# Optimization experiments

Hardware: AMD Instinct MI355X
Metric: run time of the kernel (lower is better)

Reference implementation:

```python
import jax, jax.numpy as jnp
import numpy as np

DIM = 256; K = 3; PAD = 1; DIL = 1; B = 16; H = 56; W = 56
SP = 8           # share_planes
RADIX = 2
ATTN = max(DIM * RADIX // 4, 32)   # 128
EMB = K * K * DIM // SP            # 288

def conv(x, w, pad=0, dil=1, groups=1):
    return jax.lax.conv_general_dilated(
        x, w, (1, 1), [(pad, pad), (pad, pad)], rhs_dilation=(dil, dil),
        feature_group_count=groups, dimension_numbers=('NCHW', 'OIHW', 'NCHW'))

def bn(x, g, b, m, v, eps=1e-5):
    # eval-mode BatchNorm2d
    s = g * jax.lax.rsqrt(v + eps)
    return x * s[None, :, None, None] + (b - m * s)[None, :, None, None]

def gn(x, g, b, groups, eps=1e-5):
    Bb, C, Hh, Ww = x.shape
    xg = x.reshape(Bb, groups, C // groups, Hh, Ww)
    mu = xg.mean((2, 3, 4), keepdims=True)
    var = xg.var((2, 3, 4), keepdims=True)
    xg = (xg - mu) * jax.lax.rsqrt(var + eps)
    return xg.reshape(Bb, C, Hh, Ww) * g[None, :, None, None] + b[None, :, None, None]

def unfold3(x):
    # im2col for 3x3, stride 1, pad 1 -> (B, C, K*K, H, W)
    Bb, C, Hh, Ww = x.shape
    p = (K - 1) // 2
    xp = jnp.pad(x, ((0, 0), (0, 0), (p, p), (p, p)))
    return jnp.stack([xp[:, :, i:i + Hh, j:j + Ww] for i in range(K) for j in range(K)], axis=2)

def reference(x, ke_w, ke_g, ke_b, ke_m, ke_v, e1_w, e1_g, e1_b, e1_m, e1_v,
              e2_w, e2_b, gng, gnb, c1_w, c1_g, c1_b, c1_m, c1_v,
              b2_g, b2_b, b2_m, b2_v, s1_w, s1_b, s1_g, s1_bb, s1_m, s1_v,
              s2_w, s2_b):
    Bb = x.shape[0]
    # key embed: grouped kxk conv + BN + ReLU
    k = jax.nn.relu(bn(conv(x, ke_w, pad=PAD, dil=DIL, groups=4), ke_g, ke_b, ke_m, ke_v))
    qk = jnp.concatenate([x, k], axis=1)                     # (B, 2*DIM, H, W)
    # dynamic kernel branch
    wemb = jax.nn.relu(bn(conv(qk, e1_w), e1_g, e1_b, e1_m, e1_v))
    wemb = conv(wemb, e2_w) + e2_b[None, :, None, None]
    wemb = gn(wemb, gng, gnb, DIM // SP)                     # GroupNorm(dim//8 groups)
    wemb = wemb.reshape(Bb, DIM // SP, K * K, H, W)
    # value branch
    xq = bn(conv(x, c1_w), c1_g, c1_b, c1_m, c1_v)
    # local dynamic convolution: per-pixel kernel shared across SP channels
    patches = unfold3(xq).reshape(Bb, DIM // SP, SP, K * K, H, W)
    y = (patches * wemb[:, :, None]).sum(3).reshape(Bb, DIM, H, W)
    y = bn(y, b2_g, b2_b, b2_m, b2_v)
    y = y * jax.nn.sigmoid(y)                                # swish
    # split attention over radix=2 branches (y, k)
    xs = jnp.stack([y, k], axis=2)                           # (B, C, 2, H, W)
    gap = xs.sum(2).mean((2, 3), keepdims=True)              # (B, C, 1, 1)
    a = jax.nn.relu(bn(conv(gap, s1_w) + s1_b[None, :, None, None], s1_g, s1_bb, s1_m, s1_v))
    a = conv(a, s2_w) + s2_b[None, :, None, None]            # (B, 2*C, 1, 1)
    a = jax.nn.softmax(a.reshape(Bb, DIM, RADIX), axis=2)
    out = (xs * a[:, :, :, None, None]).sum(2)
    return out

def setup_inputs():
    key = jax.random.key(0)
    ks = iter(jax.random.split(key, 40))
    def n(shape, s=1.0):
        return jax.random.normal(next(ks), shape, jnp.float32) * s
    def u(shape):
        return jax.random.uniform(next(ks), shape, jnp.float32, minval=0.5, maxval=1.5)
    d = {}
    d['x'] = n((B, DIM, H, W))
    d['ke_w'] = n((DIM, DIM // 4, K, K), 0.05)
    d['ke_g'] = u((DIM,)); d['ke_b'] = n((DIM,), 0.1); d['ke_m'] = n((DIM,), 0.1); d['ke_v'] = u((DIM,))
    d['e1_w'] = n((DIM // 2, 2 * DIM, 1, 1), 0.05)
    d['e1_g'] = u((DIM // 2,)); d['e1_b'] = n((DIM // 2,), 0.1); d['e1_m'] = n((DIM // 2,), 0.1); d['e1_v'] = u((DIM // 2,))
    d['e2_w'] = n((EMB, DIM // 2, 1, 1), 0.05); d['e2_b'] = n((EMB,), 0.1)
    d['gng'] = u((EMB,)); d['gnb'] = n((EMB,), 0.1)
    d['c1_w'] = n((DIM, DIM, 1, 1), 0.05)
    d['c1_g'] = u((DIM,)); d['c1_b'] = n((DIM,), 0.1); d['c1_m'] = n((DIM,), 0.1); d['c1_v'] = u((DIM,))
    d['b2_g'] = u((DIM,)); d['b2_b'] = n((DIM,), 0.1); d['b2_m'] = n((DIM,), 0.1); d['b2_v'] = u((DIM,))
    d['s1_w'] = n((ATTN, DIM, 1, 1), 0.05); d['s1_b'] = n((ATTN,), 0.1)
    d['s1_g'] = u((ATTN,)); d['s1_bb'] = n((ATTN,), 0.1); d['s1_m'] = n((ATTN,), 0.1); d['s1_v'] = u((ATTN,))
    d['s2_w'] = n((RADIX * DIM, ATTN, 1, 1), 0.05); d['s2_b'] = n((RADIX * DIM,), 0.1)
    return d
```

## Files before the change

### kernel.cpp

```cpp
#include <hip/hip_runtime.h>
#include <hip/hip_bf16.h>

typedef __hip_bfloat16 bf16;
typedef float f32x4 __attribute__((ext_vector_type(4)));
typedef short s16x8 __attribute__((ext_vector_type(8)));

#define NPIX 3136
#define HDIM 56
#define CDIM 256
#define PPIX 3364

static __device__ __forceinline__ float b2f(bf16 v){ return __bfloat162float(v); }
static __device__ __forceinline__ bf16  f2b(float v){ return __float2bfloat16(v); }

#define O_KE_S 0
#define O_KE_B 256
#define O_E1_S 512
#define O_E1_B 640
#define O_C1_S 768
#define O_C1_B 1024
#define O_B2_S 1280
#define O_B2_B 1536
#define O_S1_S 1792
#define O_S1_B 1920
#define O_E2B  2048
#define O_GNS  2336
#define O_GAP  3360
#define O_ATT  7456

__global__ void prep(
    const float* __restrict__ kew, const float* __restrict__ e1w,
    const float* __restrict__ e2w, const float* __restrict__ c1w,
    const float* keg, const float* keb, const float* kem, const float* kev,
    const float* e1g, const float* e1b, const float* e1m, const float* e1v,
    const float* e2b,
    const float* c1g, const float* c1b, const float* c1m, const float* c1v,
    const float* b2g, const float* b2b, const float* b2m, const float* b2v,
    const float* s1g, const float* s1bb, const float* s1m, const float* s1v,
    bf16* kewT, bf16* e1wb, bf16* e2wb, bf16* c1wb, float* o,
    bf16* xh, bf16* xq)
{
    int bid = blockIdx.x, t = threadIdx.x;
    if (bid < 576) {
        int i = bid * 256 + t;
        int ci = i & 63, co_l = (i >> 6) & 63;
        int gt = i >> 12;
        int tap = gt % 9, g = gt / 9;
        int co = g * 64 + co_l;
        kewT[i] = f2b(kew[(co * 64 + ci) * 9 + tap]);
    } else if (bid < 832) {
        int i = (bid - 576) * 256 + t; e1wb[i] = f2b(e1w[i]);
    } else if (bid < 976) {
        int i = (bid - 832) * 256 + t; e2wb[i] = f2b(e2w[i]);
    } else if (bid < 1232) {
        int i = (bid - 976) * 256 + t; c1wb[i] = f2b(c1w[i]);
    } else if (bid == 1232) {
        const float eps = 1e-5f;
        {
            float s = keg[t] * rsqrtf(kev[t] + eps);
            o[O_KE_S + t] = s; o[O_KE_B + t] = keb[t] - kem[t] * s;
            s = c1g[t] * rsqrtf(c1v[t] + eps);
            o[O_C1_S + t] = s; o[O_C1_B + t] = c1b[t] - c1m[t] * s;
            s = b2g[t] * rsqrtf(b2v[t] + eps);
            o[O_B2_S + t] = s; o[O_B2_B + t] = b2b[t] - b2m[t] * s;
        }
        if (t < 128) {
            float s = e1g[t] * rsqrtf(e1v[t] + eps);
            o[O_E1_S + t] = s; o[O_E1_B + t] = e1b[t] - e1m[t] * s;
            s = s1g[t] * rsqrtf(s1v[t] + eps);
            o[O_S1_S + t] = s; o[O_S1_B + t] = s1bb[t] - s1m[t] * s;
        }
        for (int i = t; i < 288; i += 256) o[O_E2B + i] = e2b[i];
    } else if (bid < 1253) {
        int j = (bid - 1233) * 256 + t;
        if (j < 1024) o[O_GNS + j] = 0.f;
        else if (j < 5120) o[O_GAP + j - 1024] = 0.f;
    } else {
        int j = (bid - 1253) * 256 + t;
        bf16* arr = (j >= 116736) ? xq : xh;
        int r = j % 116736;
        int img = r / 7296;
        int s = r % 7296;
        int pi = s >> 5, cc = s & 31;
        int pos;
        if (pi < 58)       pos = pi;
        else if (pi < 116) pos = 57 * 58 + (pi - 58);
        else if (pi < 172) pos = (pi - 115) * 58;
        else               pos = (pi - 171) * 58 + 57;
        float4 z = {0.f, 0.f, 0.f, 0.f};
        *(float4*)(arr + ((long)img * PPIX + pos) * 256 + cc * 8) = z;
    }
}

__global__ __launch_bounds__(256) void cvt_x(const float* __restrict__ x, bf16* __restrict__ xh)
{
    int b = blockIdx.z;
    int c0 = blockIdx.y * 64;
    int p0 = blockIdx.x * 64;
    __shared__ bf16 T[64][72];
    int t = threadIdx.x;
    #pragma unroll
    for (int it = 0; it < 4; it++) {
        int slot = t + it * 256;
        int cl = slot >> 4, ch4 = slot & 15;
        float4 v = *(const float4*)(x + ((long)b * CDIM + c0 + cl) * NPIX + p0 + ch4 * 4);
        T[ch4 * 4 + 0][cl] = f2b(v.x);
        T[ch4 * 4 + 1][cl] = f2b(v.y);
        T[ch4 * 4 + 2][cl] = f2b(v.z);
        T[ch4 * 4 + 3][cl] = f2b(v.w);
    }
    __syncthreads();
    #pragma unroll
    for (int it = 0; it < 2; it++) {
        int slot = t + it * 256;
        int p = slot >> 3, cc = slot & 7;
        int pl = p0 + p;
        int h = pl / HDIM, w = pl - h * HDIM;
        *(float4*)(xh + ((long)b * PPIX + (h + 1) * 58 + (w + 1)) * 256 + c0 + cc * 8) = *(const float4*)&T[p][cc * 8];
    }
}

__global__ __launch_bounds__(256, 4) void gconv_mfma(
    const bf16* __restrict__ xp, const bf16* __restrict__ wT,
    const float* __restrict__ scale, const float* __restrict__ bias,
    bf16* __restrict__ kh, float* __restrict__ gap)
{
    int b = blockIdx.z, g = blockIdx.y;
    int h0 = blockIdx.x * 2;
    __shared__ bf16 As[232 * 64];
    int t = threadIdx.x;
    int wv = t >> 6, lane = t & 63, q = lane >> 4, ln = lane & 15;

    #pragma unroll
    for (int i = 0; i < 8; i++) {
        int slot = t + i * 256;
        if (slot < 1856) {
            int pos = slot >> 3, chunkL = slot & 7;
            int ri = pos / 58, ci = pos - ri * 58;
            int chunkg = chunkL ^ (pos & 7);
            float4 v = *(const float4*)(xp + (((long)b * PPIX + (h0 + ri) * 58 + ci) * 256 + g * 64 + chunkg * 8));
            *(float4*)&As[pos * 64 + chunkL * 8] = v;
        }
    }

    int posb[7];
    #pragma unroll
    for (int pt = 0; pt < 7; pt++) {
        int p = pt * 16 + ln;
        int prow = (p >= 56) ? 1 : 0;
        int pcol = p - prow * 56;
        posb[pt] = prow * 58 + pcol + 1;
    }
    const bf16* wbase = wT + ((long)(g * 9) * 64 + wv * 16 + ln) * 64;

    __syncthreads();

    f32x4 acc[7] = {};
    #pragma unroll
    for (int tap = 0; tap < 9; tap++) {
        const int dr = tap / 3;
        const int dc = tap % 3 - 1;
        const bf16* wq = wbase + tap * 64 * 64;
        s16x8 B0 = *(const s16x8*)(wq + q * 8);
        s16x8 B1 = *(const s16x8*)(wq + 32 + q * 8);
        #pragma unroll
        for (int pt = 0; pt < 7; pt++) {
            int pos = posb[pt] + dr * 58 + dc;
            int off0 = pos * 64 + ((q ^ (pos & 7)) * 8);
            s16x8 a0 = *(const s16x8*)&As[off0];
            s16x8 a1 = *(const s16x8*)&As[off0 ^ 32];
            acc[pt] = __builtin_amdgcn_mfma_f32_16x16x32_bf16(a0, B0, acc[pt], 0, 0, 0);
            acc[pt] = __builtin_amdgcn_mfma_f32_16x16x32_bf16(a1, B1, acc[pt], 0, 0, 0);
        }
    }

    __syncthreads();
    bf16* T = As;
    int co = g * 64 + wv * 16 + ln;
    float sc = scale[co], bi = bias[co];
    #pragma unroll
    for (int pt = 0; pt < 7; pt++)
        #pragma unroll
        for (int r = 0; r < 4; r++)
            T[(pt * 16 + q * 4 + r) * 72 + wv * 16 + ln] = f2b(fmaxf(acc[pt][r] * sc + bi, 0.f));
    __syncthreads();
    int pimg0 = blockIdx.x * 112;
    #pragma unroll
    for (int i = 0; i < 4; i++) {
        int slot = t + i * 256;
        if (slot < 896) {
            int row = slot >> 3, cc = slot & 7;
            *(float4*)(kh + ((long)b * NPIX + pimg0 + row) * CDIM + g * 64 + cc * 8) = *(const float4*)&T[row * 72 + cc * 8];
        }
    }
    {
        int co_l = t & 63, rb = t >> 6;
        float s = 0.f;
        #pragma unroll
        for (int r = 0; r < 28; r++) s += b2f(T[(rb * 28 + r) * 72 + co_l]);
        atomicAdd(&gap[b * 256 + g * 64 + co_l], s);
    }
}

__global__ __launch_bounds__(256) void gemm_pair(
    const bf16* __restrict__ e1w, const bf16* __restrict__ c1w,
    const bf16* __restrict__ X0, const bf16* __restrict__ X1,
    const float* __restrict__ fold,
    bf16* __restrict__ Ye1, bf16* __restrict__ Yc1)
{
    int b = blockIdx.z;
    int p0 = blockIdx.x * 64;
    int by = blockIdx.y;
    const bf16* Wt; int K, M, m0; const float *scp, *bip; bf16* Y; bool relu;
    if (by == 0) { Wt = e1w; K = 512; M = 128; m0 = 0;
                   scp = fold + O_E1_S; bip = fold + O_E1_B; Y = Ye1; relu = true; }
    else         { Wt = c1w; K = 256; M = 256; m0 = (by - 1) * 128;
                   scp = fold + O_C1_S; bip = fold + O_C1_B; Y = Yc1; relu = false; }
    const int C0 = 256;

    __shared__ bf16 SH[64 * 72 + 128 * 72];
    bf16* As = SH;
    bf16* Bs = SH + 64 * 72;
    int t = threadIdx.x;
    int wv = t >> 6, lane = t & 63, q = lane >> 4, ln = lane & 15;

    f32x4 acc[4][2] = {};
    for (int k0 = 0; k0 < K; k0 += 64) {
        __syncthreads();
        #pragma unroll
        for (int i = 0; i < 2; i++) {
            int slot = t + i * 256;
            int chunk = slot & 7, row = slot >> 3;
            int ch = k0 + chunk * 8;
            const bf16* src;
            if (ch < C0) {
                long pp = p0 + row;
                long pidx = (long)b * PPIX + pp + 2 * (pp / HDIM) + 59;
                src = X0 + pidx * C0 + ch;
            } else {
                src = X1 + ((long)b * NPIX + p0 + row) * 256 + (ch - C0);
            }
            *(float4*)&As[row * 72 + chunk * 8] = *(const float4*)src;
        }
        #pragma unroll
        for (int i = 0; i < 4; i++) {
            int slot = t + i * 256;
            int chunk = slot & 7, row = slot >> 3;
            *(float4*)&Bs[row * 72 + chunk * 8] = *(const float4*)(Wt + (long)(m0 + row) * K + k0 + chunk * 8);
        }
        __syncthreads();
        #pragma unroll
        for (int kk = 0; kk < 2; kk++) {
            s16x8 a[4];
            #pragma unroll
            for (int pt = 0; pt < 4; pt++)
                a[pt] = *(const s16x8*)&As[(pt * 16 + ln) * 72 + kk * 32 + q * 8];
            #pragma unroll
            for (int mi = 0; mi < 2; mi++) {
                s16x8 bb = *(const s16x8*)&Bs[(wv * 32 + mi * 16 + ln) * 72 + kk * 32 + q * 8];
                #pragma unroll
                for (int pt = 0; pt < 4; pt++)
                    acc[pt][mi] = __builtin_amdgcn_mfma_f32_16x16x32_bf16(a[pt], bb, acc[pt][mi], 0, 0, 0);
            }
        }
    }

    __syncthreads();
    bf16* T = SH;
    #pragma unroll
    for (int mi = 0; mi < 2; mi++) {
        int m = m0 + wv * 32 + mi * 16 + ln;
        float sc = scp[m], bi = bip[m];
        #pragma unroll
        for (int pt = 0; pt < 4; pt++) {
            #pragma unroll
            for (int r = 0; r < 4; r++) {
                float v = acc[pt][mi][r] * sc + bi;
                if (relu) v = fmaxf(v, 0.f);
                T[(pt * 16 + q * 4 + r) * 144 + wv * 32 + mi * 16 + ln] = f2b(v);
            }
        }
    }
    __syncthreads();
    #pragma unroll
    for (int i = 0; i < 4; i++) {
        int slot = t + i * 256;
        int row = slot >> 4, chunk = slot & 15;
        long pp = p0 + row;
        long pidx = (by == 0) ? ((long)b * NPIX + pp)
                              : ((long)b * PPIX + pp + 2 * (pp / HDIM) + 59);
        *(float4*)(Y + pidx * M + m0 + chunk * 8) = *(const float4*)&T[row * 144 + chunk * 8];
    }
}

__global__ __launch_bounds__(256) void mfma_gemm_e2(
    const bf16* __restrict__ Wt, const bf16* __restrict__ X0,
    const float* __restrict__ bias,
    bf16* __restrict__ Y, float* __restrict__ gnsum)
{
    const int K = 128, M = 288;
    int b = blockIdx.z;
    int p0 = blockIdx.x * 64;
    int m0 = blockIdx.y * 128;
    __shared__ bf16 SH[64 * 72 + 128 * 72];
    bf16* As = SH;
    bf16* Bs = SH + 64 * 72;
    __shared__ float gs[64];
    int t = threadIdx.x;
    int wv = t >> 6, lane = t & 63, q = lane >> 4, ln = lane & 15;
    if (t < 64) gs[t] = 0.f;

    f32x4 acc[4][2] = {};
    for (int k0 = 0; k0 < K; k0 += 64) {
        __syncthreads();
        #pragma unroll
        for (int i = 0; i < 2; i++) {
            int slot = t + i * 256;
            int chunk = slot & 7, row = slot >> 3;
            int ch = k0 + chunk * 8;
            *(float4*)&As[row * 72 + chunk * 8] = *(const float4*)(X0 + ((long)b * NPIX + p0 + row) * K + ch);
        }
        #pragma unroll
        for (int i = 0; i < 4; i++) {
            int slot = t + i * 256;
            int chunk = slot & 7, row = slot >> 3;
            int m = m0 + row;
            float4 v = {0.f, 0.f, 0.f, 0.f};
            if (m < M) v = *(const float4*)(Wt + (long)m * K + k0 + chunk * 8);
            *(float4*)&Bs[row * 72 + chunk * 8] = v;
        }
        __syncthreads();
        #pragma unroll
        for (int kk = 0; kk < 2; kk++) {
            s16x8 a[4];
            #pragma unroll
            for (int pt = 0; pt < 4; pt++)
                a[pt] = *(const s16x8*)&As[(pt * 16 + ln) * 72 + kk * 32 + q * 8];
            #pragma unroll
            for (int mi = 0; mi < 2; mi++) {
                s16x8 bb = *(const s16x8*)&Bs[(wv * 32 + mi * 16 + ln) * 72 + kk * 32 + q * 8];
                #pragma unroll
                for (int pt = 0; pt < 4; pt++)
                    acc[pt][mi] = __builtin_amdgcn_mfma_f32_16x16x32_bf16(a[pt], bb, acc[pt][mi], 0, 0, 0);
            }
        }
    }

    __syncthreads();
    bf16* T = SH;
    #pragma unroll
    for (int mi = 0; mi < 2; mi++) {
        int m = m0 + wv * 32 + mi * 16 + ln;
        int mc = (m > M - 1) ? (M - 1) : m;
        float bi = bias[mc];
        float ps = 0.f, pq = 0.f;
        #pragma unroll
        for (int pt = 0; pt < 4; pt++) {
            #pragma unroll
            for (int r = 0; r < 4; r++) {
                float v = acc[pt][mi][r] + bi;
                ps += v; pq += v * v;
                T[(pt * 16 + q * 4 + r) * 144 + wv * 32 + mi * 16 + ln] = f2b(v);
            }
        }
        if (m < M) {
            int grp = m / 9;
            atomicAdd(&gs[grp * 2], ps);
            atomicAdd(&gs[grp * 2 + 1], pq);
        }
    }
    __syncthreads();
    #pragma unroll
    for (int i = 0; i < 4; i++) {
        int slot = t + i * 256;
        int chunk = slot & 15, row = slot >> 4;
        int m = m0 + chunk * 8;
        if (m + 8 <= M)
            *(float4*)(Y + ((long)b * NPIX + p0 + row) * M + m) = *(const float4*)&T[row * 144 + chunk * 8];
    }
    if (t < 64) atomicAdd(&gnsum[b * 64 + t], gs[t]);
}

__global__ __launch_bounds__(256) void dynconv(
    const bf16* __restrict__ xq, const bf16* __restrict__ wemb,
    const float* __restrict__ gnsum,
    const float* __restrict__ gng, const float* __restrict__ gnb,
    const float* __restrict__ b2s, const float* __restrict__ b2b,
    bf16* __restrict__ y, float* __restrict__ gap)
{
    int t = threadIdx.x;
    int grp = t & 31, pl = t >> 5;
    int bid = blockIdx.x;
    int b = bid / 392;
    int p0 = (bid - b * 392) * 8;
    int p = p0 + pl;
    int h = p / HDIM, w = p - h * HDIM;

    __shared__ bf16 WE[2304];
    __shared__ float SA[288], SC[288];
    __shared__ float R[8][256];

    {
        const bf16* src = wemb + (long)(b * NPIX + p0) * 288;
        #pragma unroll
        for (int i = 0; i < 2; i++) {
            int s = t + i * 256;
            if (s < 288) *(float4*)&WE[s * 8] = *(const float4*)(src + s * 8);
        }
    }
    for (int s = t; s < 288; s += 256) {
        int g2 = s / 9;
        float S = gnsum[b * 64 + g2 * 2], Q = gnsum[b * 64 + g2 * 2 + 1];
        float mu = S * (1.f / 28224.f);
        float var = Q * (1.f / 28224.f) - mu * mu;
        float rs = rsqrtf(fmaxf(var, 0.f) + 1e-5f);
        float a = rs * gng[s];
        SA[s] = a;
        SC[s] = gnb[s] - mu * a;
    }
    __syncthreads();

    long base = ((long)b * PPIX + (h + 1) * 58 + (w + 1)) * 256 + grp * 8;
    const bf16* rm = xq + base - 58 * 256;
    const bf16* rc = xq + base;
    const bf16* rq = xq + base + 58 * 256;
    s16x8 xv[9];
    xv[0] = *(const s16x8*)(rm - 256); xv[1] = *(const s16x8*)rm; xv[2] = *(const s16x8*)(rm + 256);
    xv[3] = *(const s16x8*)(rc - 256); xv[4] = *(const s16x8*)rc; xv[5] = *(const s16x8*)(rc + 256);
    xv[6] = *(const s16x8*)(rq - 256); xv[7] = *(const s16x8*)rq; xv[8] = *(const s16x8*)(rq + 256);

    float acc[8] = {};
    #pragma unroll
    for (int tp = 0; tp < 9; tp++) {
        int wi = grp * 9 + tp;
        float wt = b2f(WE[pl * 288 + wi]) * SA[wi] + SC[wi];
        const bf16* xb = (const bf16*)&xv[tp];
        #pragma unroll
        for (int i = 0; i < 8; i++) acc[i] += b2f(xb[i]) * wt;
    }

    bf16 outv[8];
    float sv[8];
    #pragma unroll
    for (int i = 0; i < 8; i++) {
        int c = grp * 8 + i;
        float v = acc[i] * b2s[c] + b2b[c];
        float sw = v / (1.f + __expf(-v));
        sv[i] = sw;
        outv[i] = f2b(sw);
    }
    *(float4*)(y + ((long)b * NPIX + p) * CDIM + grp * 8) = *(const float4*)outv;

    #pragma unroll
    for (int i = 0; i < 8; i++) R[pl][grp * 8 + i] = sv[i];
    __syncthreads();
    float s = 0.f;
    #pragma unroll
    for (int j = 0; j < 8; j++) s += R[j][t];
    atomicAdd(&gap[b * 256 + t], s);
}

__global__ void attnk(const float* __restrict__ gap,
                      const float* __restrict__ s1w, const float* __restrict__ s1b,
                      const float* __restrict__ s1s, const float* __restrict__ s1bi,
                      const float* __restrict__ s2w, const float* __restrict__ s2b,
                      float* __restrict__ att)
{
    int b = blockIdx.x, t = threadIdx.x;
    __shared__ float g[256], a1[128];
    for (int i = t; i < 256; i += 128) g[i] = gap[b * 256 + i] * (1.f / NPIX);
    __syncthreads();
    float s = 0.f;
    for (int ci = 0; ci < 256; ci++) s += s1w[t * 256 + ci] * g[ci];
    s += s1b[t];
    s = s * s1s[t] + s1bi[t];
    a1[t] = fmaxf(s, 0.f);
    __syncthreads();
    for (int c = t; c < 256; c += 128) {
        float v0 = s2b[2 * c], v1 = s2b[2 * c + 1];
        for (int ci = 0; ci < 128; ci++) {
            float av = a1[ci];
            v0 += s2w[(2 * c) * 128 + ci] * av;
            v1 += s2w[(2 * c + 1) * 128 + ci] * av;
        }
        float m = fmaxf(v0, v1);
        float e0 = __expf(v0 - m), e1 = __expf(v1 - m);
        float inv = 1.f / (e0 + e1);
        att[(b * 256 + c) * 2 + 0] = e0 * inv;
        att[(b * 256 + c) * 2 + 1] = e1 * inv;
    }
}

__global__ __launch_bounds__(256) void finalk(
    const bf16* __restrict__ y, const bf16* __restrict__ k,
    const float* __restrict__ att, float* __restrict__ out)
{
    int b = blockIdx.z, c0 = blockIdx.y * 64, p0 = blockIdx.x * 64;
    __shared__ bf16 Ys[64][72], Ks[64][72];
    int t = threadIdx.x;
    #pragma unroll
    for (int i = 0; i < 2; i++) {
        int slot = t + i * 256;
        int row = slot >> 3, cc = slot & 7;
        long off = ((long)b * NPIX + p0 + row) * CDIM + c0 + cc * 8;
        *(float4*)&Ys[row][cc * 8] = *(const float4*)(y + off);
        *(float4*)&Ks[row][cc * 8] = *(const float4*)(k + off);
    }
    __syncthreads();
    int c_l = t >> 2, pc = t & 3;
    int c = c0 + c_l;
    float a0 = att[(b * 256 + c) * 2], a1 = att[(b * 256 + c) * 2 + 1];
    float4 o[4];
    float* of = (float*)o;
    #pragma unroll
    for (int j = 0; j < 16; j++) {
        int p = pc * 16 + j;
        of[j] = b2f(Ys[p][c_l]) * a0 + b2f(Ks[p][c_l]) * a1;
    }
    float* dst = out + ((long)b * CDIM + c) * NPIX + p0 + pc * 16;
    #pragma unroll
    for (int j = 0; j < 4; j++) ((float4*)dst)[j] = o[j];
}

extern "C" void kernel_launch(void* const* d_in, const int* in_sizes, int n_in,
                              void* d_out, int out_size, void* d_ws, size_t ws_size,
                              hipStream_t stream)
{
    const float* x    = (const float*)d_in[0];
    const float* ke_w = (const float*)d_in[1];
    const float* ke_g = (const float*)d_in[2];
    const float* ke_b = (const float*)d_in[3];
    const float* ke_m = (const float*)d_in[4];
    const float* ke_v = (const float*)d_in[5];
    const float* e1_w = (const float*)d_in[6];
    const float* e1_g = (const float*)d_in[7];
    const float* e1_b = (const float*)d_in[8];
    const float* e1_m = (const float*)d_in[9];
    const float* e1_v = (const float*)d_in[10];
    const float* e2_w = (const float*)d_in[11];
    const float* e2_b = (const float*)d_in[12];
    const float* gng  = (const float*)d_in[13];
    const float* gnb  = (const float*)d_in[14];
    const float* c1_w = (const float*)d_in[15];
    const float* c1_g = (const float*)d_in[16];
    const float* c1_b = (const float*)d_in[17];
    const float* c1_m = (const float*)d_in[18];
    const float* c1_v = (const float*)d_in[19];
    const float* b2_g = (const float*)d_in[20];
    const float* b2_b = (const float*)d_in[21];
    const float* b2_m = (const float*)d_in[22];
    const float* b2_v = (const float*)d_in[23];
    const float* s1_w = (const float*)d_in[24];
    const float* s1_b = (const float*)d_in[25];
    const float* s1_g = (const float*)d_in[26];
    const float* s1_bb= (const float*)d_in[27];
    const float* s1_m = (const float*)d_in[28];
    const float* s1_v = (const float*)d_in[29];
    const float* s2_w = (const float*)d_in[30];
    const float* s2_b = (const float*)d_in[31];

    float* fold = (float*)d_ws;
    bf16* wsb   = (bf16*)((char*)d_ws + 65536);
    bf16* xh   = wsb;
    bf16* kh   = xh + 13778944L;
    bf16* wemb = kh + 12845056L;
    bf16* w1   = wemb + 14450688L;
    bf16* kewT = w1 + 6422528L;
    bf16* e1wb = kewT + 147456L;
    bf16* e2wb = e1wb + 65536L;
    bf16* c1wb = e2wb + 36864L;
    bf16* xq   = c1wb + 65536L;
    bf16* yb   = xh;

    prep<<<dim3(2165), dim3(256), 0, stream>>>(
        ke_w, e1_w, e2_w, c1_w,
        ke_g, ke_b, ke_m, ke_v, e1_g, e1_b, e1_m, e1_v, e2_b,
        c1_g, c1_b, c1_m, c1_v, b2_g, b2_b, b2_m, b2_v,
        s1_g, s1_bb, s1_m, s1_v,
        kewT, e1wb, e2wb, c1wb, fold, xh, xq);

    cvt_x<<<dim3(49, 4, 16), dim3(256), 0, stream>>>(x, xh);

    gconv_mfma<<<dim3(28, 4, 16), dim3(256), 0, stream>>>(
        xh, kewT, fold + O_KE_S, fold + O_KE_B, kh, fold + O_GAP);

    gemm_pair<<<dim3(49, 3, 16), dim3(256), 0, stream>>>(
        e1wb, c1wb, xh, kh, fold, w1, xq);

    mfma_gemm_e2<<<dim3(49, 3, 16), dim3(256), 0, stream>>>(
        e2wb, w1, fold + O_E2B, wemb, fold + O_GNS);

    dynconv<<<dim3(6272), dim3(256), 0, stream>>>(
        xq, wemb, fold + O_GNS, gng, gnb,
        fold + O_B2_S, fold + O_B2_B, yb, fold + O_GAP);

    attnk<<<dim3(16), dim3(128), 0, stream>>>(
        fold + O_GAP, s1_w, s1_b, fold + O_S1_S, fold + O_S1_B, s2_w, s2_b, fold + O_ATT);

    finalk<<<dim3(49, 4, 16), dim3(256), 0, stream>>>(yb, kh, fold + O_ATT, (float*)d_out);
}
```

Baseline: 352.5 us.

## Co-schedule grouped conv with c1 GEMM and precompute GroupNorm fold

Merges the grouped 3x3 key conv and the independent c1 1x1 GEMM into one launch, with block-index ranges selecting which role each block plays, so the two run concurrently and fill the GPU better. The e1 GEMM becomes its own specialised kernel. GroupNorm scale/shift is now computed once per batch in a small gnfold kernel rather than recomputed by each of the 6272 dynconv blocks. This adds one extra launch and moves the workspace offset to make room for the folded values. The heterogeneous blocks may also unbalance the schedule.

New measurement: 333.0 us. -5.5%, faster.

```diff
diff --git a/kernel.cpp b/kernel.cpp
--- a/kernel.cpp
+++ b/kernel.cpp
@@ -27,6 +27,7 @@
 #define O_GNS  2336
 #define O_GAP  3360
 #define O_ATT  7456
+#define O_SA   15872
 
 __global__ void prep(
     const float* __restrict__ kew, const float* __restrict__ e1w,
@@ -120,104 +121,164 @@
     }
 }
 
-__global__ __launch_bounds__(256, 4) void gconv_mfma(
+__global__ __launch_bounds__(256) void gconv_c1(
     const bf16* __restrict__ xp, const bf16* __restrict__ wT,
-    const float* __restrict__ scale, const float* __restrict__ bias,
-    bf16* __restrict__ kh, float* __restrict__ gap)
-{
-    int b = blockIdx.z, g = blockIdx.y;
-    int h0 = blockIdx.x * 2;
-    __shared__ bf16 As[232 * 64];
+    const float* __restrict__ kes, const float* __restrict__ keb,
+    const bf16* __restrict__ c1w,
+    const float* __restrict__ c1s, const float* __restrict__ c1b,
+    bf16* __restrict__ kh, bf16* __restrict__ xq, float* __restrict__ gap)
+{
+    __shared__ bf16 SH[232 * 64];
+    int b = blockIdx.z;
+    int bx = blockIdx.x;
     int t = threadIdx.x;
     int wv = t >> 6, lane = t & 63, q = lane >> 4, ln = lane & 15;
 
-    #pragma unroll
-    for (int i = 0; i < 8; i++) {
-        int slot = t + i * 256;
-        if (slot < 1856) {
-            int pos = slot >> 3, chunkL = slot & 7;
-            int ri = pos / 58, ci = pos - ri * 58;
-            int chunkg = chunkL ^ (pos & 7);
-            float4 v = *(const float4*)(xp + (((long)b * PPIX + (h0 + ri) * 58 + ci) * 256 + g * 64 + chunkg * 8));
-            *(float4*)&As[pos * 64 + chunkL * 8] = v;
-        }
-    }
-
-    int posb[7];
-    #pragma unroll
-    for (int pt = 0; pt < 7; pt++) {
-        int p = pt * 16 + ln;
-        int prow = (p >= 56) ? 1 : 0;
-        int pcol = p - prow * 56;
-        posb[pt] = prow * 58 + pcol + 1;
-    }
-    const bf16* wbase = wT + ((long)(g * 9) * 64 + wv * 16 + ln) * 64;
-
-    __syncthreads();
-
-    f32x4 acc[7] = {};
-    #pragma unroll
-    for (int tap = 0; tap < 9; tap++) {
-        const int dr = tap / 3;
-        const int dc = tap % 3 - 1;
-        const bf16* wq = wbase + tap * 64 * 64;
-        s16x8 B0 = *(const s16x8*)(wq + q * 8);
-        s16x8 B1 = *(const s16x8*)(wq + 32 + q * 8);
+    if (bx < 112) {
+        int hx = bx >> 2, g = bx & 3;
+        int h0 = hx * 2;
+        bf16* As = SH;
+        #pragma unroll
+        for (int i = 0; i < 8; i++) {
+            int slot = t + i * 256;
+            if (slot < 1856) {
+                int pos = slot >> 3, chunkL = slot & 7;
+                int ri = pos / 58, ci = pos - ri * 58;
+                int chunkg = chunkL ^ (pos & 7);
+                float4 v = *(const float4*)(xp + (((long)b * PPIX + (h0 + ri) * 58 + ci) * 256 + g * 64 + chunkg * 8));
+                *(float4*)&As[pos * 64 + chunkL * 8] = v;
+            }
+        }
+        int posb[7];
         #pragma unroll
         for (int pt = 0; pt < 7; pt++) {
-            int pos = posb[pt] + dr * 58 + dc;
-            int off0 = pos * 64 + ((q ^ (pos & 7)) * 8);
-            s16x8 a0 = *(const s16x8*)&As[off0];
-            s16x8 a1 = *(const s16x8*)&As[off0 ^ 32];
-            acc[pt] = __builtin_amdgcn_mfma_f32_16x16x32_bf16(a0, B0, acc[pt], 0, 0, 0);
-            acc[pt] = __builtin_amdgcn_mfma_f32_16x16x32_bf16(a1, B1, acc[pt], 0, 0, 0);
-        }
-    }
-
-    __syncthreads();
-    bf16* T = As;
-    int co = g * 64 + wv * 16 + ln;
-    float sc = scale[co], bi = bias[co];
-    #pragma unroll
-    for (int pt = 0; pt < 7; pt++)
-        #pragma unroll
-        for (int r = 0; r < 4; r++)
-            T[(pt * 16 + q * 4 + r) * 72 + wv * 16 + ln] = f2b(fmaxf(acc[pt][r] * sc + bi, 0.f));
-    __syncthreads();
-    int pimg0 = blockIdx.x * 112;
-    #pragma unroll
-    for (int i = 0; i < 4; i++) {
-        int slot = t + i * 256;
-        if (slot < 896) {
-            int row = slot >> 3, cc = slot & 7;
-            *(float4*)(kh + ((long)b * NPIX + pimg0 + row) * CDIM + g * 64 + cc * 8) = *(const float4*)&T[row * 72 + cc * 8];
-        }
-    }
-    {
-        int co_l = t & 63, rb = t >> 6;
-        float s = 0.f;
-        #pragma unroll
-        for (int r = 0; r < 28; r++) s += b2f(T[(rb * 28 + r) * 72 + co_l]);
-        atomicAdd(&gap[b * 256 + g * 64 + co_l], s);
-    }
-}
-
-__global__ __launch_bounds__(256) void gemm_pair(
-    const bf16* __restrict__ e1w, const bf16* __restrict__ c1w,
-    const bf16* __restrict__ X0, const bf16* __restrict__ X1,
-    const float* __restrict__ fold,
-    bf16* __restrict__ Ye1, bf16* __restrict__ Yc1)
-{
-    int b = blockIdx.z;
+            int p = pt * 16 + ln;
+            int prow = (p >= 56) ? 1 : 0;
+            int pcol = p - prow * 56;
+            posb[pt] = prow * 58 + pcol + 1;
+        }
+        const bf16* wbase = wT + ((long)(g * 9) * 64 + wv * 16 + ln) * 64;
+        __syncthreads();
+
+        f32x4 acc[7] = {};
+        #pragma unroll
+        for (int tap = 0; tap < 9; tap++) {
+            const int dr = tap / 3;
+            const int dc = tap % 3 - 1;
+            const bf16* wq = wbase + tap * 64 * 64;
+            s16x8 B0 = *(const s16x8*)(wq + q * 8);
+            s16x8 B1 = *(const s16x8*)(wq + 32 + q * 8);
+            #pragma unroll
+            for (int pt = 0; pt < 7; pt++) {
+                int pos = posb[pt] + dr * 58 + dc;
+                int off0 = pos * 64 + ((q ^ (pos & 7)) * 8);
+                s16x8 a0 = *(const s16x8*)&As[off0];
+                s16x8 a1 = *(const s16x8*)&As[off0 ^ 32];
+                acc[pt] = __builtin_amdgcn_mfma_f32_16x16x32_bf16(a0, B0, acc[pt], 0, 0, 0);
+                acc[pt] = __builtin_amdgcn_mfma_f32_16x16x32_bf16(a1, B1, acc[pt], 0, 0, 0);
+            }
+        }
+        __syncthreads();
+        bf16* T = As;
+        int co = g * 64 + wv * 16 + ln;
+        float sc = kes[co], bi = keb[co];
+        #pragma unroll
+        for (int pt = 0; pt < 7; pt++)
+            #pragma unroll
+            for (int r = 0; r < 4; r++)
+                T[(pt * 16 + q * 4 + r) * 72 + wv * 16 + ln] = f2b(fmaxf(acc[pt][r] * sc + bi, 0.f));
+        __syncthreads();
+        int pimg0 = hx * 112;
+        #pragma unroll
+        for (int i = 0; i < 4; i++) {
+            int slot = t + i * 256;
+            if (slot < 896) {
+                int row = slot >> 3, cc = slot & 7;
+                *(float4*)(kh + ((long)b * NPIX + pimg0 + row) * CDIM + g * 64 + cc * 8) = *(const float4*)&T[row * 72 + cc * 8];
+            }
+        }
+        {
+            int co_l = t & 63, rb = t >> 6;
+            float s = 0.f;
+            #pragma unroll
+            for (int r = 0; r < 28; r++) s += b2f(T[(rb * 28 + r) * 72 + co_l]);
+            atomicAdd(&gap[b * 256 + g * 64 + co_l], s);
+        }
+    } else {
+        int px = bx - 112;
+        int mt = px & 1; px >>= 1;
+        int p0 = px * 64;
+        int m0 = mt * 128;
+        bf16* As = SH;
+        bf16* Bs = SH + 64 * 72;
+
+        f32x4 acc[4][2] = {};
+        for (int k0 = 0; k0 < 256; k0 += 64) {
+            __syncthreads();
+            #pragma unroll
+            for (int i = 0; i < 2; i++) {
+                int slot = t + i * 256;
+                int chunk = slot & 7, row = slot >> 3;
+                long pp = p0 + row;
+                long pidx = (long)b * PPIX + pp + 2 * (pp / HDIM) + 59;
+                *(float4*)&As[row * 72 + chunk * 8] = *(const float4*)(xp + pidx * 256 + k0 + chunk * 8);
+            }
+            #pragma unroll
+            for (int i = 0; i < 4; i++) {
+                int slot = t + i * 256;
+                int chunk = slot & 7, row = slot >> 3;
+                *(float4*)&Bs[row * 72 + chunk * 8] = *(const float4*)(c1w + (long)(m0 + row) * 256 + k0 + chunk * 8);
+            }
+            __syncthreads();
+            #pragma unroll
+            for (int kk = 0; kk < 2; kk++) {
+                s16x8 a[4];
+                #pragma unroll
+                for (int pt = 0; pt < 4; pt++)
+                    a[pt] = *(const s16x8*)&As[(pt * 16 + ln) * 72 + kk * 32 + q * 8];
+                #pragma unroll
+                for (int mi = 0; mi < 2; mi++) {
+                    s16x8 bb = *(const s16x8*)&Bs[(wv * 32 + mi * 16 + ln) * 72 + kk * 32 + q * 8];
+                    #pragma unroll
+                    for (int pt = 0; pt < 4; pt++)
+                        acc[pt][mi] = __builtin_amdgcn_mfma_f32_16x16x32_bf16(a[pt], bb, acc[pt][mi], 0, 0, 0);
+                }
+            }
+        }
+        __syncthreads();
+        bf16* T = SH;
+        #pragma unroll
+        for (int mi = 0; mi < 2; mi++) {
+            int m = m0 + wv * 32 + mi * 16 + ln;
+            float sc = c1s[m], bi = c1b[m];
+            #pragma unroll
+            for (int pt = 0; pt < 4; pt++) {
+                #pragma unroll
+                for (int r = 0; r < 4; r++) {
+                    float v = acc[pt][mi][r] * sc + bi;
+                    T[(pt * 16 + q * 4 + r) * 144 + wv * 32 + mi * 16 + ln] = f2b(v);
+                }
+            }
+        }
+        __syncthreads();
+        #pragma unroll
+        for (int i = 0; i < 4; i++) {
+            int slot = t + i * 256;
+            int row = slot >> 4, chunk = slot & 15;
+            long pp = p0 + row;
+            long pidx = (long)b * PPIX + pp + 2 * (pp / HDIM) + 59;
+            *(float4*)(xq + pidx * 256 + m0 + chunk * 8) = *(const float4*)&T[row * 144 + chunk * 8];
+        }
+    }
+}
+
+__global__ __launch_bounds__(256) void mfma_gemm_e1(
+    const bf16* __restrict__ Wt, const bf16* __restrict__ X0, const bf16* __restrict__ X1,
+    const float* __restrict__ scale, const float* __restrict__ bias,
+    bf16* __restrict__ Y)
+{
+    int b = blockIdx.y;
     int p0 = blockIdx.x * 64;
-    int by = blockIdx.y;
-    const bf16* Wt; int K, M, m0; const float *scp, *bip; bf16* Y; bool relu;
-    if (by == 0) { Wt = e1w; K = 512; M = 128; m0 = 0;
-                   scp = fold + O_E1_S; bip = fold + O_E1_B; Y = Ye1; relu = true; }
-    else         { Wt = c1w; K = 256; M = 256; m0 = (by - 1) * 128;
-                   scp = fold + O_C1_S; bip = fold + O_C1_B; Y = Yc1; relu = false; }
-    const int C0 = 256;
-
     __shared__ bf16 SH[64 * 72 + 128 * 72];
     bf16* As = SH;
     bf16* Bs = SH + 64 * 72;
@@ -225,7 +286,7 @@
     int wv = t >> 6, lane = t & 63, q = lane >> 4, ln = lane & 15;
 
     f32x4 acc[4][2] = {};
-    for (int k0 = 0; k0 < K; k0 += 64) {
+    for (int k0 = 0; k0 < 512; k0 += 64) {
         __syncthreads();
         #pragma unroll
         for (int i = 0; i < 2; i++) {
@@ -233,12 +294,12 @@
             int chunk = slot & 7, row = slot >> 3;
             int ch = k0 + chunk * 8;
             const bf16* src;
-            if (ch < C0) {
+            if (ch < 256) {
                 long pp = p0 + row;
                 long pidx = (long)b * PPIX + pp + 2 * (pp / HDIM) + 59;
-                src = X0 + pidx * C0 + ch;
+                src = X0 + pidx * 256 + ch;
             } else {
-                src = X1 + ((long)b * NPIX + p0 + row) * 256 + (ch - C0);
+                src = X1 + ((long)b * NPIX + p0 + row) * 256 + (ch - 256);
             }
             *(float4*)&As[row * 72 + chunk * 8] = *(const float4*)src;
         }
@@ -246,7 +307,7 @@
         for (int i = 0; i < 4; i++) {
             int slot = t + i * 256;
             int chunk = slot & 7, row = slot >> 3;
-            *(float4*)&Bs[row * 72 + chunk * 8] = *(const float4*)(Wt + (long)(m0 + row) * K + k0 + chunk * 8);
+            *(float4*)&Bs[row * 72 + chunk * 8] = *(const float4*)(Wt + (long)row * 512 + k0 + chunk * 8);
         }
         __syncthreads();
         #pragma unroll
@@ -264,20 +325,18 @@
             }
         }
     }
-
     __syncthreads();
     bf16* T = SH;
     #pragma unroll
     for (int mi = 0; mi < 2; mi++) {
-        int m = m0 + wv * 32 + mi * 16 + ln;
-        float sc = scp[m], bi = bip[m];
+        int m = wv * 32 + mi * 16 + ln;
+        float sc = scale[m], bi = bias[m];
         #pragma unroll
         for (int pt = 0; pt < 4; pt++) {
             #pragma unroll
             for (int r = 0; r < 4; r++) {
-                float v = acc[pt][mi][r] * sc + bi;
-                if (relu) v = fmaxf(v, 0.f);
-                T[(pt * 16 + q * 4 + r) * 144 + wv * 32 + mi * 16 + ln] = f2b(v);
+                float v = fmaxf(acc[pt][mi][r] * sc + bi, 0.f);
+                T[(pt * 16 + q * 4 + r) * 144 + m] = f2b(v);
             }
         }
     }
@@ -286,10 +345,7 @@
     for (int i = 0; i < 4; i++) {
         int slot = t + i * 256;
         int row = slot >> 4, chunk = slot & 15;
-        long pp = p0 + row;
-        long pidx = (by == 0) ? ((long)b * NPIX + pp)
-                              : ((long)b * PPIX + pp + 2 * (pp / HDIM) + 59);
-        *(float4*)(Y + pidx * M + m0 + chunk * 8) = *(const float4*)&T[row * 144 + chunk * 8];
+        *(float4*)(Y + ((long)b * NPIX + p0 + row) * 128 + chunk * 8) = *(const float4*)&T[row * 144 + chunk * 8];
     }
 }
 
@@ -381,10 +437,26 @@
     if (t < 64) atomicAdd(&gnsum[b * 64 + t], gs[t]);
 }
 
+__global__ void gnfold(const float* __restrict__ gnsum,
+                       const float* __restrict__ gng, const float* __restrict__ gnb,
+                       float* __restrict__ o)
+{
+    int b = blockIdx.x, t = threadIdx.x;
+    for (int s = t; s < 288; s += 256) {
+        int g2 = s / 9;
+        float S = gnsum[b * 64 + g2 * 2], Q = gnsum[b * 64 + g2 * 2 + 1];
+        float mu = S * (1.f / 28224.f);
+        float var = Q * (1.f / 28224.f) - mu * mu;
+        float rs = rsqrtf(fmaxf(var, 0.f) + 1e-5f);
+        float a = rs * gng[s];
+        o[O_SA + b * 576 + s] = a;
+        o[O_SA + b * 576 + 288 + s] = gnb[s] - mu * a;
+    }
+}
+
 __global__ __launch_bounds__(256) void dynconv(
     const bf16* __restrict__ xq, const bf16* __restrict__ wemb,
-    const float* __restrict__ gnsum,
-    const float* __restrict__ gng, const float* __restrict__ gnb,
+    const float* __restrict__ fold,
     const float* __restrict__ b2s, const float* __restrict__ b2b,
     bf16* __restrict__ y, float* __restrict__ gap)
 {
@@ -397,7 +469,7 @@
     int h = p / HDIM, w = p - h * HDIM;
 
     __shared__ bf16 WE[2304];
-    __shared__ float SA[288], SC[288];
+    __shared__ float SAB[576];
     __shared__ float R[8][256];
 
     {
@@ -408,15 +480,9 @@
             if (s < 288) *(float4*)&WE[s * 8] = *(const float4*)(src + s * 8);
         }
     }
-    for (int s = t; s < 288; s += 256) {
-        int g2 = s / 9;
-        float S = gnsum[b * 64 + g2 * 2], Q = gnsum[b * 64 + g2 * 2 + 1];
-        float mu = S * (1.f / 28224.f);
-        float var = Q * (1.f / 28224.f) - mu * mu;
-        float rs = rsqrtf(fmaxf(var, 0.f) + 1e-5f);
-        float a = rs * gng[s];
-        SA[s] = a;
-        SC[s] = gnb[s] - mu * a;
+    {
+        const float4* src = (const float4*)(fold + O_SA + b * 576);
+        if (t < 144) ((float4*)SAB)[t] = src[t];
     }
     __syncthreads();
 
@@ -433,7 +499,7 @@
     #pragma unroll
     for (int tp = 0; tp < 9; tp++) {
         int wi = grp * 9 + tp;
-        float wt = b2f(WE[pl * 288 + wi]) * SA[wi] + SC[wi];
+        float wt = b2f(WE[pl * 288 + wi]) * SAB[wi] + SAB[288 + wi];
         const bf16* xb = (const bf16*)&xv[tp];
         #pragma unroll
         for (int i = 0; i < 8; i++) acc[i] += b2f(xb[i]) * wt;
@@ -560,7 +626,7 @@
     const float* s2_b = (const float*)d_in[31];
 
     float* fold = (float*)d_ws;
-    bf16* wsb   = (bf16*)((char*)d_ws + 65536);
+    bf16* wsb   = (bf16*)((char*)d_ws + 131072);
     bf16* xh   = wsb;
     bf16* kh   = xh + 13778944L;
     bf16* wemb = kh + 12845056L;
@@ -581,18 +647,21 @@
 
     cvt_x<<<dim3(49, 4, 16), dim3(256), 0, stream>>>(x, xh);
 
-    gconv_mfma<<<dim3(28, 4, 16), dim3(256), 0, stream>>>(
-        xh, kewT, fold + O_KE_S, fold + O_KE_B, kh, fold + O_GAP);
-
-    gemm_pair<<<dim3(49, 3, 16), dim3(256), 0, stream>>>(
-        e1wb, c1wb, xh, kh, fold, w1, xq);
+    gconv_c1<<<dim3(210, 1, 16), dim3(256), 0, stream>>>(
+        xh, kewT, fold + O_KE_S, fold + O_KE_B,
+        c1wb, fold + O_C1_S, fold + O_C1_B,
+        kh, xq, fold + O_GAP);
+
+    mfma_gemm_e1<<<dim3(49, 16), dim3(256), 0, stream>>>(
+        e1wb, xh, kh, fold + O_E1_S, fold + O_E1_B, w1);
 
     mfma_gemm_e2<<<dim3(49, 3, 16), dim3(256), 0, stream>>>(
         e2wb, w1, fold + O_E2B, wemb, fold + O_GNS);
 
+    gnfold<<<dim3(16), dim3(256), 0, stream>>>(fold + O_GNS, gng, gnb, fold);
+
     dynconv<<<dim3(6272), dim3(256), 0, stream>>>(
-        xq, wemb, fold + O_GNS, gng, gnb,
-        fold + O_B2_S, fold + O_B2_B, yb, fold + O_GAP);
+        xq, wemb, fold, fold + O_B2_S, fold + O_B2_B, yb, fold + O_GAP);
 
     attnk<<<dim3(16), dim3(128), 0, stream>>>(
         fold + O_GAP, s1_w, s1_b, fold + O_S1_S, fold + O_S1_B, s2_w, s2_b, fold + O_ATT);
```
